# Kernel optimization log

Hardware: AMD Instinct MI355X
Metric: run time of the kernel (lower is better)

The kernel has to match this reference:

```python
import jax, jax.numpy as jnp
import numpy as np
from jax import lax


def setup_inputs() -> dict:
    T, L = 2048, 1024
    key = jax.random.key(0)
    k1, k2, k3 = jax.random.split(key, 3)
    feats = jax.random.normal(k1, (T, L), dtype=jnp.float32)
    transfer = jax.random.normal(k2, (L, L), dtype=jnp.float32)
    target = jax.random.randint(k3, (T,), 0, L)
    return {"feats": feats, "transfer": transfer, "target": target, "input_length": T}


def reference(feats, transfer, target, input_length):
    # CRF loss = log Z (forward algorithm) - gold path score.
    # feats: [T, L] emission scores, transfer: [L, L] transition scores
    # (transfer[i, j] = score of moving from label i to label j).

    def step(prev_scores, emit):
        # prev_scores: [L]; emit: [L]
        # scores[j] = logsumexp_i(prev[i] + transfer[i, j]) + emit[j]
        new_scores = jax.nn.logsumexp(prev_scores[:, None] + transfer, axis=0) + emit
        return new_scores, None

    init = feats[0]                      # scores[0] = feats[0]
    final, _ = lax.scan(step, init, feats[1:])
    log_z = jax.nn.logsumexp(final)

    # Gold score: emissions along the target path + transitions between
    # consecutive target labels.
    T = feats.shape[0]
    emit_score = jnp.sum(feats[jnp.arange(T), target])
    trans_score = jnp.sum(transfer[target[:-1], target[1:]])
    gold = emit_score + trans_score

    return log_z - gold
```

## Files before the change

kernel.cpp:

```cpp
#include <hip/hip_runtime.h>
#include <stdint.h>

#define T_LEN 2048
#define L     1024
#define TPBW  1024
#define NCB   16
#define COLS  64
#define GOLDW 32
#define TMID  1023
#define BSTEPS 1024
#define SPIN_MAX (1 << 14)

#define NFB   64
#define CPB   16
#define TPB   256

#define SCOPE_AGENT __HIP_MEMORY_SCOPE_AGENT
#define LDA(p) __hip_atomic_load((p), __ATOMIC_RELAXED, SCOPE_AGENT)
#define STA(p, v) __hip_atomic_store((p), (v), __ATOMIC_RELAXED, SCOPE_AGENT)

__device__ __forceinline__ uint64_t pack_su(int tag, float v) {
    return ((uint64_t)(uint32_t)tag << 32) | (uint64_t)__float_as_uint(v);
}

__global__ __launch_bounds__(TPBW, 1)
void crf_v4(const float* __restrict__ feats,
            const float* __restrict__ transfer,
            const int* __restrict__ target,
            float* __restrict__ out,
            uint64_t* __restrict__ ws64)
{
    __shared__ __align__(16) float qbuf[2][L];
    __shared__ float red[32];
    __shared__ float sh_shift;

    uint64_t* fb0 = ws64;
    uint64_t* fb1 = ws64 + L;
    uint64_t* bb0 = ws64 + 2 * L;
    uint64_t* bb1 = ws64 + 3 * L;
    uint64_t* goldslot = ws64 + 4 * L;
    (void)fb0;

    const int bid  = blockIdx.x;
    const int tid  = threadIdx.x;
    const int lane = tid & 63;
    const int wv   = tid >> 6;
    const int cl   = 2 * (lane & 1) + ((lane >> 1) & 1);

    if (bid == GOLDW) {
        float s = 0.f;
        for (int t = tid; t < T_LEN; t += TPBW)
            s += feats[t * L + target[t]];
        for (int t = tid; t < T_LEN - 1; t += TPBW)
            s += transfer[target[t] * L + target[t + 1]];
        #pragma unroll
        for (int m = 32; m; m >>= 1) s += __shfl_xor(s, m, 64);
        if (lane == 0) red[wv] = s;
        __syncthreads();
        if (tid == 0) {
            float g = 0.f;
            #pragma unroll
            for (int i = 0; i < 16; ++i) g += red[i];
            STA(goldslot, pack_su(1, g));
        }
        return;
    }

    if (bid < NCB) {
        const int role    = bid;
        const int colbase = role * COLS;
        const int gcb     = colbase + 4 * wv;

        float E[16][4];
        #pragma unroll
        for (int k = 0; k < 16; ++k) {
            const float4 r = *(const float4*)(transfer + (size_t)(lane + 64 * k) * L + gcb);
            E[k][0] = __expf(r.x); E[k][1] = __expf(r.y);
            E[k][2] = __expf(r.z); E[k][3] = __expf(r.w);
        }

        for (int t = 1; t <= TMID; ++t) {
            const int par = t & 1;
            const uint64_t* rbuf = par ? fb0 : fb1;
            uint64_t* wbuf = par ? fb1 : fb0;
            const int expect = t - 1;

            const float fe = feats[(size_t)t * L + gcb + cl];

            float val, sloc;
            if (t == 1) {
                val  = feats[tid];
                sloc = feats[colbase];
            } else {
                sloc = sh_shift;
                const uint64_t* p = rbuf + tid;
                uint64_t v;
                int n = 0;
                do { v = LDA(p); } while ((int)(v >> 32) < expect && ++n < SPIN_MAX);
                val = __uint_as_float((uint32_t)v);
            }

            float* qb = qbuf[par];
            qb[tid] = __expf(val - sloc);
            __syncthreads();

            float a0 = 0.f, a1 = 0.f, a2 = 0.f, a3 = 0.f;
            #pragma unroll
            for (int k = 0; k < 16; ++k) {
                const float q = qb[lane + 64 * k];
                a0 += q * E[k][0]; a1 += q * E[k][1];
                a2 += q * E[k][2]; a3 += q * E[k][3];
            }

            {
                const bool h1 = lane & 1;
                float s0 = h1 ? a0 : a2;  float r0 = __shfl_xor(s0, 1, 64);
                float s1 = h1 ? a1 : a3;  float r1 = __shfl_xor(s1, 1, 64);
                a0 = (h1 ? a2 : a0) + r0;
                a1 = (h1 ? a3 : a1) + r1;
                const bool h2 = lane & 2;
                float s2 = h2 ? a0 : a1;  float r2 = __shfl_xor(s2, 2, 64);
                a0 = (h2 ? a1 : a0) + r2;
            }
            float s = a0;
            s += __shfl_xor(s, 4, 64);
            s += __shfl_xor(s, 8, 64);
            s += __shfl_xor(s, 16, 64);
            s += __shfl_xor(s, 32, 64);

            const float nv = sloc + __logf(s) + fe;
            if (lane < 4)
                STA(&wbuf[gcb + cl], pack_su(t, nv));
            if (tid == 0) sh_shift = nv;
            __syncthreads();
        }

        if (role == 0) {
            const uint64_t* fp = fb1 + tid;
            const uint64_t* bp = bb0 + tid;
            uint64_t fv_, bv_;
            int n = 0;
            for (;;) {
                fv_ = LDA(fp); bv_ = LDA(bp);
                bool ready = ((int)(fv_ >> 32) >= TMID) & ((int)(bv_ >> 32) >= BSTEPS);
                if (ready || ++n >= SPIN_MAX) break;
            }
            const float sv = __uint_as_float((uint32_t)fv_) + __uint_as_float((uint32_t)bv_);
            float mx = sv;
            #pragma unroll
            for (int m = 32; m; m >>= 1) mx = fmaxf(mx, __shfl_xor(mx, m, 64));
            if (lane == 0) red[wv] = mx;
            __syncthreads();
            float M = red[0];
            #pragma unroll
            for (int i = 1; i < 16; ++i) M = fmaxf(M, red[i]);
            float sm = __expf(sv - M);
            #pragma unroll
            for (int m = 32; m; m >>= 1) sm += __shfl_xor(sm, m, 64);
            if (lane == 0) red[16 + wv] = sm;
            __syncthreads();
            if (tid == 0) {
                float S = 0.f;
                #pragma unroll
                for (int i = 0; i < 16; ++i) S += red[16 + i];
                const float lse = M + __logf(S);
                uint64_t g = LDA(goldslot);
                int n2 = 0;
                while ((int)(g >> 32) < 1 && ++n2 < SPIN_MAX) g = LDA(goldslot);
                out[0] = lse - __uint_as_float((uint32_t)g);
            }
        }
        return;
    }

    if (bid < 2 * NCB) {
        const int role    = bid - NCB;
        const int rowbase = role * COLS + 4 * wv;

        float E[16][4];
        #pragma unroll
        for (int r = 0; r < 4; ++r) {
            const float* rowp = transfer + (size_t)(rowbase + r) * L + lane;
            #pragma unroll
            for (int k = 0; k < 16; ++k)
                E[k][r] = __expf(rowp[64 * k]);
        }

        for (int s = 1; s <= BSTEPS; ++s) {
            const int par = s & 1;
            const uint64_t* rbuf = par ? bb0 : bb1;
            uint64_t* wbuf = par ? bb1 : bb0;
            const int expect = s - 1;
            const int t = T_LEN - s;

            const float fvv = feats[(size_t)t * L + tid];

            float bval, sb;
            if (s == 1) {
                bval = 0.f; sb = 0.f;
            } else {
                sb = sh_shift;
                const uint64_t* p = rbuf + tid;
                uint64_t v;
                int n = 0;
                do { v = LDA(p); } while ((int)(v >> 32) < expect && ++n < SPIN_MAX);
                bval = __uint_as_float((uint32_t)v);
            }

            float* qb = qbuf[par];
            qb[tid] = __expf(fvv + bval - sb);
            __syncthreads();

            float a0 = 0.f, a1 = 0.f, a2 = 0.f, a3 = 0.f;
            #pragma unroll
            for (int k = 0; k < 16; ++k) {
                const float w = qb[lane + 64 * k];
                a0 += w * E[k][0]; a1 += w * E[k][1];
                a2 += w * E[k][2]; a3 += w * E[k][3];
            }

            {
                const bool h1 = lane & 1;
                float s0 = h1 ? a0 : a2;  float r0 = __shfl_xor(s0, 1, 64);
                float s1 = h1 ? a1 : a3;  float r1 = __shfl_xor(s1, 1, 64);
                a0 = (h1 ? a2 : a0) + r0;
                a1 = (h1 ? a3 : a1) + r1;
                const bool h2 = lane & 2;
                float s2 = h2 ? a0 : a1;  float r2 = __shfl_xor(s2, 2, 64);
                a0 = (h2 ? a1 : a0) + r2;
            }
            float sum = a0;
            sum += __shfl_xor(sum, 4, 64);
            sum += __shfl_xor(sum, 8, 64);
            sum += __shfl_xor(sum, 16, 64);
            sum += __shfl_xor(sum, 32, 64);

            const float nb = sb + __logf(sum);
            if (lane < 4)
                STA(&wbuf[rowbase + cl], pack_su(s, nb));
            if (tid == 0) sh_shift = nb;
            __syncthreads();
        }
        return;
    }
}

__global__ __launch_bounds__(TPB, 1)
void crf_single(const float* __restrict__ feats,
                const float* __restrict__ transfer,
                const int* __restrict__ target,
                float* __restrict__ out,
                uint64_t* __restrict__ ws64)
{
    __shared__ __align__(16) float qbuf[2][L];
    __shared__ float red[8];

    uint64_t* buf0 = ws64;
    uint64_t* buf1 = ws64 + L;
    uint64_t* goldslot = ws64 + 2 * L;

    const int b   = blockIdx.x;
    const int tid = threadIdx.x;
    const int lane = tid & 63;
    const int wv   = tid >> 6;
    const int cl   = 2 * (lane & 1) + ((lane >> 1) & 1);

    if (b == NFB) {
        float s = 0.f;
        for (int t = tid; t < T_LEN; t += TPB)
            s += feats[t * L + target[t]];
        for (int t = tid; t < T_LEN - 1; t += TPB)
            s += transfer[target[t] * L + target[t + 1]];
        #pragma unroll
        for (int m = 32; m; m >>= 1) s += __shfl_xor(s, m, 64);
        if (lane == 0) red[wv] = s;
        __syncthreads();
        if (tid == 0) {
            float g = red[0] + red[1] + red[2] + red[3];
            STA(goldslot, pack_su(1, g));
        }
        return;
    }

    const int gcb    = b * CPB + 4 * wv;
    const int shslot = b * CPB;

    float E[16][4];
    #pragma unroll
    for (int k = 0; k < 16; ++k) {
        const float4 r = *(const float4*)(transfer + (size_t)(lane + 64 * k) * L + gcb);
        E[k][0] = __expf(r.x); E[k][1] = __expf(r.y);
        E[k][2] = __expf(r.z); E[k][3] = __expf(r.w);
    }

    if (tid < CPB) {
        int j = b * CPB + tid;
        STA(&buf0[j], pack_su(0, feats[j]));
    }

    for (int t = 1; t < T_LEN; ++t) {
        uint64_t* rbuf = (t & 1) ? buf0 : buf1;
        uint64_t* wbuf = (t & 1) ? buf1 : buf0;
        const int expect = t - 1;
        const float fe = feats[(size_t)t * L + gcb + cl];

        const uint64_t* rp = rbuf + 4 * tid;
        uint64_t v0, v1, v2, v3, vs;
        int n = 0;
        for (;;) {
            v0 = LDA(rp + 0); v1 = LDA(rp + 1);
            v2 = LDA(rp + 2); v3 = LDA(rp + 3);
            vs = LDA(rbuf + shslot);
            bool ready = ((int)(v0 >> 32) >= expect) & ((int)(v1 >> 32) >= expect) &
                         ((int)(v2 >> 32) >= expect) & ((int)(v3 >> 32) >= expect) &
                         ((int)(vs >> 32) >= expect);
            if (ready || ++n >= SPIN_MAX) break;
        }
        const float sloc = __uint_as_float((uint32_t)vs);

        float* qb = qbuf[t & 1];
        float4 qv;
        qv.x = __expf(__uint_as_float((uint32_t)v0) - sloc);
        qv.y = __expf(__uint_as_float((uint32_t)v1) - sloc);
        qv.z = __expf(__uint_as_float((uint32_t)v2) - sloc);
        qv.w = __expf(__uint_as_float((uint32_t)v3) - sloc);
        ((float4*)qb)[tid] = qv;
        __syncthreads();

        float a0 = 0.f, a1 = 0.f, a2 = 0.f, a3 = 0.f;
        #pragma unroll
        for (int k = 0; k < 16; ++k) {
            const float q = qb[lane + 64 * k];
            a0 += q * E[k][0]; a1 += q * E[k][1];
            a2 += q * E[k][2]; a3 += q * E[k][3];
        }
        {
            const bool h1 = lane & 1;
            float s0 = h1 ? a0 : a2;  float r0 = __shfl_xor(s0, 1, 64);
            float s1 = h1 ? a1 : a3;  float r1 = __shfl_xor(s1, 1, 64);
            a0 = (h1 ? a2 : a0) + r0;
            a1 = (h1 ? a3 : a1) + r1;
            const bool h2 = lane & 2;
            float s2 = h2 ? a0 : a1;  float r2 = __shfl_xor(s2, 2, 64);
            a0 = (h2 ? a1 : a0) + r2;
        }
        float s = a0;
        s += __shfl_xor(s, 4, 64);
        s += __shfl_xor(s, 8, 64);
        s += __shfl_xor(s, 16, 64);
        s += __shfl_xor(s, 32, 64);

        const float nv = sloc + __logf(s) + fe;
        if (lane < 4)
            STA(&wbuf[gcb + cl], pack_su(t, nv));
    }

    if (b == 0) {
        const uint64_t* fp = buf1 + 4 * tid;
        uint64_t v0, v1, v2, v3;
        int n = 0;
        for (;;) {
            v0 = LDA(fp + 0); v1 = LDA(fp + 1);
            v2 = LDA(fp + 2); v3 = LDA(fp + 3);
            bool ready = ((int)(v0 >> 32) >= T_LEN - 1) & ((int)(v1 >> 32) >= T_LEN - 1) &
                         ((int)(v2 >> 32) >= T_LEN - 1) & ((int)(v3 >> 32) >= T_LEN - 1);
            if (ready || ++n >= SPIN_MAX) break;
        }
        float sv[4] = { __uint_as_float((uint32_t)v0), __uint_as_float((uint32_t)v1),
                        __uint_as_float((uint32_t)v2), __uint_as_float((uint32_t)v3) };
        float mx = fmaxf(fmaxf(sv[0], sv[1]), fmaxf(sv[2], sv[3]));
        #pragma unroll
        for (int m = 32; m; m >>= 1) mx = fmaxf(mx, __shfl_xor(mx, m, 64));
        if (lane == 0) red[wv] = mx;
        __syncthreads();
        const float M = fmaxf(fmaxf(red[0], red[1]), fmaxf(red[2], red[3]));
        float sm = 0.f;
        #pragma unroll
        for (int k = 0; k < 4; ++k) sm += __expf(sv[k] - M);
        #pragma unroll
        for (int m = 32; m; m >>= 1) sm += __shfl_xor(sm, m, 64);
        if (lane == 0) red[4 + wv] = sm;
        __syncthreads();
        if (tid == 0) {
            const float S = red[4] + red[5] + red[6] + red[7];
            const float lse = M + __logf(S);
            uint64_t g = LDA(goldslot);
            int n2 = 0;
            while ((int)(g >> 32) < 1 && ++n2 < SPIN_MAX) g = LDA(goldslot);
            out[0] = lse - __uint_as_float((uint32_t)g);
        }
    }
}

extern "C" void kernel_launch(void* const* d_in, const int* in_sizes, int n_in,
                              void* d_out, int out_size, void* d_ws, size_t ws_size,
                              hipStream_t stream) {
    const float* feats    = (const float*)d_in[0];
    const float* transfer = (const float*)d_in[1];
    const int*   target   = (const int*)d_in[2];
    float* out = (float*)d_out;
    uint64_t* ws64 = (uint64_t*)d_ws;

    if (ws_size >= (4 * L + 1) * sizeof(uint64_t)) {
        hipLaunchKernelGGL(crf_v4, dim3(GOLDW + 1), dim3(TPBW), 0, stream,
                           feats, transfer, target, out, ws64);
    } else {
        hipLaunchKernelGGL(crf_single, dim3(NFB + 1), dim3(TPB), 0, stream,
                           feats, transfer, target, out, ws64);
    }
}
```

Baseline: 1.679 ms.

## Replace per-step block barriers with per-wave shared-memory ready flags

Drops both __syncthreads per time step in the forward and backward recurrences. Each wave now publishes a release flag after writing its slice of the q buffer, and consumers acquire-spin on each other wave's flag before reading that slice. The shift value is no longer broadcast through shared memory; it is read directly from element 0 of the global exchange buffer, which every block now uses as the common shift. This aims to cut barrier latency on the serial critical path, but it adds spin loads, an extra global load per poll, and removes the unrolling of the inner loop. Safety against overwriting the double-buffered qbuf relies on the global step dependency.

```diff
diff --git a/kernel.cpp b/kernel.cpp
--- a/kernel.cpp
+++ b/kernel.cpp
@@ -16,6 +16,7 @@
 #define TPB   256
 
 #define SCOPE_AGENT __HIP_MEMORY_SCOPE_AGENT
+#define SCOPE_WG    __HIP_MEMORY_SCOPE_WORKGROUP
 #define LDA(p) __hip_atomic_load((p), __ATOMIC_RELAXED, SCOPE_AGENT)
 #define STA(p, v) __hip_atomic_store((p), (v), __ATOMIC_RELAXED, SCOPE_AGENT)
 
@@ -24,22 +25,21 @@
 }
 
 __global__ __launch_bounds__(TPBW, 1)
-void crf_v4(const float* __restrict__ feats,
+void crf_v5(const float* __restrict__ feats,
             const float* __restrict__ transfer,
             const int* __restrict__ target,
             float* __restrict__ out,
             uint64_t* __restrict__ ws64)
 {
     __shared__ __align__(16) float qbuf[2][L];
+    __shared__ int   ready[2][16];
     __shared__ float red[32];
-    __shared__ float sh_shift;
 
     uint64_t* fb0 = ws64;
     uint64_t* fb1 = ws64 + L;
     uint64_t* bb0 = ws64 + 2 * L;
     uint64_t* bb1 = ws64 + 3 * L;
     uint64_t* goldslot = ws64 + 4 * L;
-    (void)fb0;
 
     const int bid  = blockIdx.x;
     const int tid  = threadIdx.x;
@@ -66,6 +66,9 @@
         return;
     }
 
+    if (tid < 32) ready[tid >> 4][tid & 15] = 0;
+    __syncthreads();
+
     if (bid < NCB) {
         const int role    = bid;
         const int colbase = role * COLS;
@@ -90,23 +93,32 @@
             float val, sloc;
             if (t == 1) {
                 val  = feats[tid];
-                sloc = feats[colbase];
+                sloc = feats[0];
             } else {
-                sloc = sh_shift;
                 const uint64_t* p = rbuf + tid;
-                uint64_t v;
+                uint64_t v, v0;
                 int n = 0;
-                do { v = LDA(p); } while ((int)(v >> 32) < expect && ++n < SPIN_MAX);
-                val = __uint_as_float((uint32_t)v);
+                for (;;) {
+                    v = LDA(p); v0 = LDA(rbuf);
+                    bool ok = ((int)(v >> 32) >= expect) & ((int)(v0 >> 32) >= expect);
+                    if (ok || ++n >= SPIN_MAX) break;
+                }
+                val  = __uint_as_float((uint32_t)v);
+                sloc = __uint_as_float((uint32_t)v0);
             }
 
             float* qb = qbuf[par];
             qb[tid] = __expf(val - sloc);
-            __syncthreads();
+            if (lane == 0)
+                __hip_atomic_store(&ready[par][wv], t, __ATOMIC_RELEASE, SCOPE_WG);
 
             float a0 = 0.f, a1 = 0.f, a2 = 0.f, a3 = 0.f;
-            #pragma unroll
             for (int k = 0; k < 16; ++k) {
+                if (k != wv) {
+                    int n2 = 0;
+                    while (__hip_atomic_load(&ready[par][k], __ATOMIC_ACQUIRE, SCOPE_WG) < t
+                           && ++n2 < SPIN_MAX) {}
+                }
                 const float q = qb[lane + 64 * k];
                 a0 += q * E[k][0]; a1 += q * E[k][1];
                 a2 += q * E[k][2]; a3 += q * E[k][3];
@@ -131,8 +143,6 @@
             const float nv = sloc + __logf(s) + fe;
             if (lane < 4)
                 STA(&wbuf[gcb + cl], pack_su(t, nv));
-            if (tid == 0) sh_shift = nv;
-            __syncthreads();
         }
 
         if (role == 0) {
@@ -142,8 +152,8 @@
             int n = 0;
             for (;;) {
                 fv_ = LDA(fp); bv_ = LDA(bp);
-                bool ready = ((int)(fv_ >> 32) >= TMID) & ((int)(bv_ >> 32) >= BSTEPS);
-                if (ready || ++n >= SPIN_MAX) break;
+                bool ok = ((int)(fv_ >> 32) >= TMID) & ((int)(bv_ >> 32) >= BSTEPS);
+                if (ok || ++n >= SPIN_MAX) break;
             }
             const float sv = __uint_as_float((uint32_t)fv_) + __uint_as_float((uint32_t)bv_);
             float mx = sv;
@@ -199,21 +209,30 @@
             if (s == 1) {
                 bval = 0.f; sb = 0.f;
             } else {
-                sb = sh_shift;
                 const uint64_t* p = rbuf + tid;
-                uint64_t v;
+                uint64_t v, v0;
                 int n = 0;
-                do { v = LDA(p); } while ((int)(v >> 32) < expect && ++n < SPIN_MAX);
+                for (;;) {
+                    v = LDA(p); v0 = LDA(rbuf);
+                    bool ok = ((int)(v >> 32) >= expect) & ((int)(v0 >> 32) >= expect);
+                    if (ok || ++n >= SPIN_MAX) break;
+                }
                 bval = __uint_as_float((uint32_t)v);
+                sb   = __uint_as_float((uint32_t)v0);
             }
 
             float* qb = qbuf[par];
             qb[tid] = __expf(fvv + bval - sb);
-            __syncthreads();
+            if (lane == 0)
+                __hip_atomic_store(&ready[par][wv], s, __ATOMIC_RELEASE, SCOPE_WG);
 
             float a0 = 0.f, a1 = 0.f, a2 = 0.f, a3 = 0.f;
-            #pragma unroll
             for (int k = 0; k < 16; ++k) {
+                if (k != wv) {
+                    int n2 = 0;
+                    while (__hip_atomic_load(&ready[par][k], __ATOMIC_ACQUIRE, SCOPE_WG) < s
+                           && ++n2 < SPIN_MAX) {}
+                }
                 const float w = qb[lane + 64 * k];
                 a0 += w * E[k][0]; a1 += w * E[k][1];
                 a2 += w * E[k][2]; a3 += w * E[k][3];
@@ -238,8 +257,6 @@
             const float nb = sb + __logf(sum);
             if (lane < 4)
                 STA(&wbuf[rowbase + cl], pack_su(s, nb));
-            if (tid == 0) sh_shift = nb;
-            __syncthreads();
         }
         return;
     }
@@ -402,7 +419,7 @@
     uint64_t* ws64 = (uint64_t*)d_ws;
 
     if (ws_size >= (4 * L + 1) * sizeof(uint64_t)) {
-        hipLaunchKernelGGL(crf_v4, dim3(GOLDW + 1), dim3(TPBW), 0, stream,
+        hipLaunchKernelGGL(crf_v5, dim3(GOLDW + 1), dim3(TPBW), 0, stream,
                            feats, transfer, target, out, ws64);
     } else {
         hipLaunchKernelGGL(crf_single, dim3(NFB + 1), dim3(TPB), 0, stream,
```

After: 3.761 ms. 2.24x slower.
